# Kernel tuning notes

Measured on AMD Instinct MI355X. Metric: run time of the kernel, lower is better.

Reference implementation:

```python
import jax, jax.numpy as jnp
from jax import lax
import numpy as np

EPS_COS = 1e-8   # cosine-similarity eps (matches F.cosine_similarity default scale)
EPS_IN = 1e-5    # InstanceNorm2d default eps
NEG = -1e9


def _conv3(x, w, b):
    # x: [B,C,H,W], w: [O,I,3,3]
    y = lax.conv_general_dilated(x, w, (1, 1), 'SAME',
                                 dimension_numbers=('NCHW', 'OIHW', 'NCHW'))
    return y + b[None, :, None, None]


def _inorm(x):
    m = jnp.mean(x, axis=(2, 3), keepdims=True)
    v = jnp.var(x, axis=(2, 3), keepdims=True)
    return (x - m) * lax.rsqrt(v + EPS_IN)


def _shift(former, latter, mask):
    # former/latter: [B,C,H,W]; mask: [H,W] int (1 = hole).
    # For every masked pixel, find the most cosine-similar UNMASKED pixel in the
    # latter (known-region encoder) features and copy the former feature from it.
    B, C, H, W = former.shape
    L = H * W
    lat = lax.stop_gradient(latter).reshape(B, C, L)           # attention is non-differentiable
    latn = lat / (jnp.linalg.norm(lat, axis=1, keepdims=True) + EPS_COS)
    sim = jnp.einsum('bcm,bcn->bmn', latn, latn)               # [B,L,L] query m -> key n
    mflat = mask.reshape(L) > 0
    sim = jnp.where(mflat[None, None, :], NEG, sim)            # keys must be unmasked
    idx = jnp.argmax(sim, axis=-1)                             # [B,L]
    fflat = former.reshape(B, C, L)
    gathered = jnp.take_along_axis(fflat, jnp.broadcast_to(idx[:, None, :], (B, C, L)), axis=2)
    shift = jnp.where(mflat[None, None, :], gathered, 0.0)     # zeros outside the hole
    return shift.reshape(B, C, H, W)


def setup_inputs() -> dict:
    key = jax.random.key(0)
    ks = jax.random.split(key, 6)
    B, C, H, W = 8, 256, 64, 64
    inp = jax.random.normal(ks[0], (B, 2 * C, H, W), dtype=jnp.float32)
    mask = jax.random.randint(ks[1], (H, W), 0, 2, dtype=jnp.int32)
    s1 = 1.0 / float(np.sqrt(2 * C * 9))
    s2 = 1.0 / float(np.sqrt(C * 9))
    W1 = jax.random.uniform(ks[2], (C, 2 * C, 3, 3), jnp.float32, -s1, s1)
    b1 = jax.random.uniform(ks[3], (C,), jnp.float32, -s1, s1)
    W2 = jax.random.uniform(ks[4], (C, C, 3, 3), jnp.float32, -s2, s2)
    b2 = jax.random.uniform(ks[5], (C,), jnp.float32, -s2, s2)
    return {"input": inp, "mask": mask, "W1": W1, "b1": b1, "W2": W2, "b2": b2}


def reference(input, mask, W1, b1, W2, b2):
    C = input.shape[1] // 2
    F_c = input[:, :C]          # former (decoder) features
    F_s = input[:, C:]          # latter (encoder) features
    F_shift = _shift(F_c, F_s, mask)
    F_fuse = F_c * F_shift
    F_com = jnp.concatenate([F_c, F_fuse], axis=1)             # [B,2C,H,W]
    h = jax.nn.relu(_inorm(_conv3(F_com, W1, b1)))
    res = _inorm(_conv3(h, W2, b2))
    return jnp.concatenate([F_c + res, F_s], axis=1)
```

## Files before the change

kernel.cpp:

```cpp
#include <hip/hip_runtime.h>
#include <hip/hip_bf16.h>
#include <math.h>

#define L 4096
#define C 256
#define B 8

typedef __attribute__((ext_vector_type(8))) short bf16x8;
typedef __attribute__((ext_vector_type(8))) ushort u16x8;
typedef __attribute__((ext_vector_type(4))) float f32x4;

__device__ inline ushort f2bu(float f) { __hip_bfloat16 h = __float2bfloat16(f); return *(ushort*)&h; }
__device__ inline float bu2f(ushort u) { __hip_bfloat16 h; *(ushort*)&h = u; return __bfloat162float(h); }

__global__ __launch_bounds__(256) void compact_mask(
    const int* __restrict__ mask, int* __restrict__ counts,
    int* __restrict__ maskedOrig, int* __restrict__ unmaskOrig,
    int* __restrict__ posOf)
{
    __shared__ int smM[256], smU[256];
    int t = threadIdx.x;
    int flags[16];
    int cm = 0, cu = 0;
    for (int k = 0; k < 16; ++k) {
        int l = t * 16 + k;
        int f = mask[l] > 0;
        flags[k] = f;
        cm += f; cu += !f;
    }
    smM[t] = cm; smU[t] = cu;
    __syncthreads();
    for (int off = 1; off < 256; off <<= 1) {
        int vM = 0, vU = 0;
        if (t >= off) { vM = smM[t - off]; vU = smU[t - off]; }
        __syncthreads();
        smM[t] += vM; smU[t] += vU;
        __syncthreads();
    }
    if (t == 255) { counts[0] = smM[255]; counts[1] = smU[255]; }
    int pm = smM[t] - cm, pu = smU[t] - cu;
    for (int k = 0; k < 16; ++k) {
        int l = t * 16 + k;
        if (flags[k]) { maskedOrig[pm] = l; posOf[l] = pm; pm++; }
        else          { unmaskOrig[pu] = l; posOf[l] = pu; pu++; }
    }
}

__global__ __launch_bounds__(256) void norm_transpose(
    const float* __restrict__ input, const int* __restrict__ mask,
    const int* __restrict__ counts, const int* __restrict__ posOf,
    ushort* __restrict__ fsnh, ushort* __restrict__ fsnl)
{
    int bx = blockIdx.x;
    int b = bx >> 7;
    int l0 = (bx & 127) * 32;
    __shared__ float tile[256 * 33];
    __shared__ float part[8 * 33];
    __shared__ float denom[32];
    __shared__ int   rowdst[32];
    int t = threadIdx.x;
    int lsub = t & 31, cg = t >> 5;
    for (int cc = 0; cc < 256; cc += 8) {
        int c = cc + cg;
        tile[c * 33 + lsub] = input[((size_t)(b * 512 + 256 + c)) * L + l0 + lsub];
    }
    __syncthreads();
    float s = 0.f;
    for (int c = cg; c < 256; c += 8) { float v = tile[c * 33 + lsub]; s = fmaf(v, v, s); }
    part[cg * 33 + lsub] = s;
    __syncthreads();
    if (t < 32) {
        float s2 = 0.f;
        for (int g = 0; g < 8; ++g) s2 += part[g * 33 + t];
        denom[t] = sqrtf(s2) + 1e-8f;
        int l = l0 + t;
        int Nm = counts[0];
        rowdst[t] = (mask[l] > 0) ? posOf[l] : (Nm + posOf[l]);
    }
    __syncthreads();
    for (int ls = 0; ls < 32; ++ls) {
        int r = rowdst[ls];
        float d = denom[ls];
        float val = tile[t * 33 + ls] / d;
        ushort h = f2bu(val);
        float hf = bu2f(h);
        ushort lo = f2bu(val - hf);
        size_t o = ((size_t)b * L + r) * C + t;
        fsnh[o] = h;
        fsnl[o] = lo;
    }
}

__global__ __launch_bounds__(512, 1) void sim_argmax_v3(
    const ushort* __restrict__ hi, const ushort* __restrict__ lo,
    const int* __restrict__ counts,
    float* __restrict__ pval, int* __restrict__ pidx)
{
    __shared__ ushort ldsB[65536];
    const int Nm = counts[0], Nu = counts[1];
    const int b = blockIdx.z;
    const int m0 = blockIdx.y * 64;
    const int half = blockIdx.x;
    const int t = threadIdx.x;
    const int w = t >> 6, l = t & 63;
    const int lm = l & 15, lk = l >> 4;
    const int mh = w & 1, nq = w >> 1;

    const int nct = (Nu + 63) >> 6;
    const int hs = (nct + 1) >> 1;
    const int cA = half * hs, cB = half ? nct : hs;

    float bestv0[4], bestv1[4]; int bestn0[4], bestn1[4];
#pragma unroll
    for (int r = 0; r < 4; ++r) {
        bestv0[r] = -3e38f; bestn0[r] = 0;
        bestv1[r] = -3e38f; bestn1[r] = 0;
    }

    if (m0 >= Nm) return;

    if (cA < cB) {
        char* ldsc = (char*)ldsB;
        const char* bytesH = (const char*)hi;
        const char* bytesL = (const char*)lo;
        const size_t bL = (size_t)b * L;

#define STAGE(bufofs, cc) do { \
    size_t gb = (bL + (size_t)Nm + (size_t)(cc) * 64) * 512; \
    _Pragma("unroll") \
    for (int i = 0; i < 4; ++i) { \
        int xu = w * 4096 + i * 1024; \
        int xl = xu + l * 16; \
        int sx = xl ^ (((xl >> 9) & 7) << 4); \
        __builtin_amdgcn_global_load_lds((const __attribute__((address_space(1))) unsigned*)(bytesH + gb + sx), \
            (__attribute__((address_space(3))) unsigned*)(ldsc + (bufofs) + xu), 16, 0, 0); \
        __builtin_amdgcn_global_load_lds((const __attribute__((address_space(1))) unsigned*)(bytesL + gb + sx), \
            (__attribute__((address_space(3))) unsigned*)(ldsc + (bufofs) + 32768 + xu), 16, 0, 0); \
    } \
} while (0)

        STAGE(0, cA);

        const int rA0 = m0 + mh * 32 + lm;
        bf16x8 ah0[8], al0[8], ah1[8], al1[8];
        {
            const ushort* aH0 = hi + (bL + rA0) * C + lk * 8;
            const ushort* aL0 = lo + (bL + rA0) * C + lk * 8;
            const ushort* aH1 = aH0 + 16 * C;
            const ushort* aL1 = aL0 + 16 * C;
#pragma unroll
            for (int ks = 0; ks < 8; ++ks) {
                ah0[ks] = *(const bf16x8*)(aH0 + ks * 32);
                al0[ks] = *(const bf16x8*)(aL0 + ks * 32);
                ah1[ks] = *(const bf16x8*)(aH1 + ks * 32);
                al1[ks] = *(const bf16x8*)(aL1 + ks * 32);
            }
        }

        const int row = nq * 16 + lm;
        const int key = (row & 7) << 4;

        for (int c = cA; c < cB; ++c) {
            int bo = ((c - cA) & 1) * 65536;
            asm volatile("s_waitcnt vmcnt(0)" ::: "memory");
            __syncthreads();
            if (c + 1 < cB) STAGE(bo ^ 65536, c + 1);
            const char* bhp = ldsc + bo + row * 512;
            const char* blp = bhp + 32768;
            f32x4 acc0 = (f32x4){0.f, 0.f, 0.f, 0.f};
            f32x4 acc1 = (f32x4){0.f, 0.f, 0.f, 0.f};
#pragma unroll
            for (int ks = 0; ks < 8; ++ks) {
                int off = (ks * 64 + lk * 16) ^ key;
                bf16x8 bh = *(const bf16x8*)(bhp + off);
                bf16x8 bl = *(const bf16x8*)(blp + off);
                acc0 = __builtin_amdgcn_mfma_f32_16x16x32_bf16(ah0[ks], bh, acc0, 0, 0, 0);
                acc0 = __builtin_amdgcn_mfma_f32_16x16x32_bf16(ah0[ks], bl, acc0, 0, 0, 0);
                acc0 = __builtin_amdgcn_mfma_f32_16x16x32_bf16(al0[ks], bh, acc0, 0, 0, 0);
                acc1 = __builtin_amdgcn_mfma_f32_16x16x32_bf16(ah1[ks], bh, acc1, 0, 0, 0);
                acc1 = __builtin_amdgcn_mfma_f32_16x16x32_bf16(ah1[ks], bl, acc1, 0, 0, 0);
                acc1 = __builtin_amdgcn_mfma_f32_16x16x32_bf16(al1[ks], bh, acc1, 0, 0, 0);
            }
            int n = c * 64 + nq * 16 + lm;
            bool nv = n < Nu;
#pragma unroll
            for (int r = 0; r < 4; ++r) {
                float v0 = acc0[r];
                if (nv && v0 > bestv0[r]) { bestv0[r] = v0; bestn0[r] = n; }
                float v1 = acc1[r];
                if (nv && v1 > bestv1[r]) { bestv1[r] = v1; bestn1[r] = n; }
            }
        }
#undef STAGE
    }

#pragma unroll
    for (int r = 0; r < 4; ++r) {
        float bv = bestv0[r]; int bn = bestn0[r];
#pragma unroll
        for (int mk = 1; mk < 16; mk <<= 1) {
            float ov = __shfl_xor(bv, mk, 64);
            int   on = __shfl_xor(bn, mk, 64);
            if (ov > bv || (ov == bv && on < bn)) { bv = ov; bn = on; }
        }
        if (lm == 0) {
            int m = m0 + mh * 32 + lk * 4 + r;
            size_t o = ((size_t)(b * 4096 + m)) * 8 + half * 4 + nq;
            pval[o] = bv; pidx[o] = bn;
        }
        bv = bestv1[r]; bn = bestn1[r];
#pragma unroll
        for (int mk = 1; mk < 16; mk <<= 1) {
            float ov = __shfl_xor(bv, mk, 64);
            int   on = __shfl_xor(bn, mk, 64);
            if (ov > bv || (ov == bv && on < bn)) { bv = ov; bn = on; }
        }
        if (lm == 0) {
            int m = m0 + mh * 32 + 16 + lk * 4 + r;
            size_t o = ((size_t)(b * 4096 + m)) * 8 + half * 4 + nq;
            pval[o] = bv; pidx[o] = bn;
        }
    }
}

__global__ __launch_bounds__(256) void argmax_reduce8(
    const float* __restrict__ pval, const int* __restrict__ pidx,
    const int* __restrict__ counts, const int* __restrict__ maskedOrig,
    const int* __restrict__ unmaskOrig, int* __restrict__ idxmap)
{
    int i = blockIdx.x * 256 + threadIdx.x;
    int b = i >> 12, m = i & 4095;
    if (m >= counts[0]) return;
    size_t base = (size_t)i * 8;
    float bv = pval[base]; int bn = pidx[base];
#pragma unroll
    for (int p = 1; p < 8; ++p) {
        float v = pval[base + p]; int n2 = pidx[base + p];
        if (v > bv || (v == bv && n2 < bn)) { bv = v; bn = n2; }
    }
    idxmap[(b << 12) + maskedOrig[m]] = unmaskOrig[bn];
}

__global__ __launch_bounds__(256) void wprep(
    const float* __restrict__ W1, const float* __restrict__ W2,
    ushort* __restrict__ W1bf, ushort* __restrict__ W2bf)
{
    int gid = blockIdx.x * 256 + threadIdx.x;
    const int N1 = 256 * 512 * 9;
    const int N2 = 256 * 256 * 9;
    if (gid < N1) {
        int ci = gid & 511; int rest = gid >> 9;
        int tau = rest % 9; int co = rest / 9;
        W1bf[gid] = f2bu(W1[((size_t)(co * 512 + ci)) * 9 + tau]);
    } else if (gid < N1 + N2) {
        int g = gid - N1;
        int ci = g & 255; int rest = g >> 8;
        int tau = rest % 9; int co = rest / 9;
        W2bf[g] = f2bu(W2[((size_t)(co * 256 + ci)) * 9 + tau]);
    }
}

__global__ __launch_bounds__(256) void in_prep1(
    const float* __restrict__ input, ushort* __restrict__ inT)
{
    int b = blockIdx.y;
    int p0 = blockIdx.x * 32;
    __shared__ float tile[256][33];
    int t = threadIdx.x;
    int pq = t & 7;
    for (int cc = 0; cc < 256; cc += 32) {
        int ci = cc + (t >> 3);
        float4 v = *(const float4*)(input + ((size_t)(b * 512 + ci)) * L + p0 + pq * 4);
        tile[ci][pq * 4 + 0] = v.x; tile[ci][pq * 4 + 1] = v.y;
        tile[ci][pq * 4 + 2] = v.z; tile[ci][pq * 4 + 3] = v.w;
    }
    __syncthreads();
    int c8 = t & 31;
    for (int pp = 0; pp < 32; pp += 8) {
        int pixloc = pp + (t >> 5);
        u16x8 u;
#pragma unroll
        for (int j = 0; j < 8; ++j) u[j] = f2bu(tile[c8 * 8 + j][pixloc]);
        *(u16x8*)(inT + ((size_t)(b * 4096 + p0 + pixloc)) * 512 + c8 * 8) = u;
    }
}

__global__ __launch_bounds__(256) void in_prep2(
    ushort* __restrict__ inT, const int* __restrict__ mask,
    const int* __restrict__ idxmap)
{
    int gid = blockIdx.x * 256 + threadIdx.x;
    int c8 = gid & 31;
    int pix = (gid >> 5) & 4095;
    int b = gid >> 17;
    u16x8 out8;
    if (mask[pix] > 0) {
        int n = idxmap[(b << 12) + pix];
        const ushort* rp = inT + ((size_t)(b * 4096 + pix)) * 512 + c8 * 8;
        const ushort* rn = inT + ((size_t)(b * 4096 + n)) * 512 + c8 * 8;
        u16x8 a = *(const u16x8*)rp;
        u16x8 bb = *(const u16x8*)rn;
#pragma unroll
        for (int j = 0; j < 8; ++j) out8[j] = f2bu(bu2f(a[j]) * bu2f(bb[j]));
    } else {
#pragma unroll
        for (int j = 0; j < 8; ++j) out8[j] = 0;
    }
    *(u16x8*)(inT + ((size_t)(b * 4096 + pix)) * 512 + 256 + c8 * 8) = out8;
}

template<int CKROW>
__global__ __launch_bounds__(256, 2) void conv_mfma(
    const ushort* __restrict__ Abf, const ushort* __restrict__ Wbf,
    float* __restrict__ outF, ushort* __restrict__ outH,
    float* __restrict__ psum, int store32)
{
    __shared__ float4 ldsv[62208 / 16];
    char* lds = (char*)ldsv;
    char* ldsB = lds + 25344;
    const int t = threadIdx.x;
    const int w = t >> 6;
    const int l = t & 63;
    const int lm = l & 15, lk = l >> 4;
    const int b = blockIdx.z;
    const int y0 = blockIdx.x * 4;
    const int c0 = blockIdx.y * 64;
    const int yw = y0 + w;
    const size_t abase = (size_t)b * 4096 * CKROW;

    f32x4 acc[4][4];
#pragma unroll
    for (int g = 0; g < 4; ++g)
#pragma unroll
        for (int nf = 0; nf < 4; ++nf) acc[g][nf] = (f32x4){0.f, 0.f, 0.f, 0.f};

    if (t < 48) {
        int r = t >> 3;
        int cX = ((t >> 2) & 1) ? 65 : 0;
        int k8 = t & 3;
        *(float4*)(lds + (r * 66 + cX) * 64 + ((k8 * 16) ^ ((cX & 3) << 4))) = (float4){0.f,0.f,0.f,0.f};
    }

    const int NKC = CKROW / 32;
    for (int kc = 0; kc < NKC; ++kc) {
        __syncthreads();
        {
            int x = t >> 2;
            int k8 = t & 3;
            int cX = x + 1;
            char* dbase = lds + cX * 64 + ((k8 * 16) ^ ((cX & 3) << 4));
#pragma unroll
            for (int r = 0; r < 6; ++r) {
                int yy = y0 - 1 + r;
                float4 v;
                if (yy >= 0 && yy < 64)
                    v = *(const float4*)(Abf + abase + (size_t)(yy * 64 + x) * CKROW + kc * 32 + k8 * 8);
                else
                    v = (float4){0.f, 0.f, 0.f, 0.f};
                *(float4*)(dbase + r * (66 * 64)) = v;
            }
        }
        {
            int cl = t >> 2;
            int k8 = t & 3;
            char* dbase = ldsB + cl * 64 + ((k8 * 16) ^ ((cl & 3) << 4));
            const ushort* sbase = Wbf + ((size_t)(c0 + cl) * 9) * CKROW + kc * 32 + k8 * 8;
#pragma unroll
            for (int tau = 0; tau < 9; ++tau) {
                *(float4*)(dbase + tau * (64 * 64)) = *(const float4*)(sbase + (size_t)tau * CKROW);
            }
        }
        __syncthreads();
#pragma unroll
        for (int ky = 0; ky < 3; ++ky) {
            int r = w + ky;
#pragma unroll
            for (int kx = 0; kx < 3; ++kx) {
                int tau = ky * 3 + kx;
                bf16x8 bfr[4];
#pragma unroll
                for (int nf = 0; nf < 4; ++nf) {
                    int cl = nf * 16 + lm;
                    bfr[nf] = *(bf16x8*)(ldsB + (tau * 64 + cl) * 64 + ((lk * 16) ^ ((cl & 3) << 4)));
                }
#pragma unroll
                for (int g = 0; g < 4; ++g) {
                    int cX = g * 16 + lm + kx;
                    bf16x8 afr = *(bf16x8*)(lds + (r * 66 + cX) * 64 + ((lk * 16) ^ ((cX & 3) << 4)));
#pragma unroll
                    for (int nf = 0; nf < 4; ++nf)
                        acc[g][nf] = __builtin_amdgcn_mfma_f32_16x16x32_bf16(afr, bfr[nf], acc[g][nf], 0, 0, 0);
                }
            }
        }
    }

    if (store32) {
#pragma unroll
        for (int g = 0; g < 4; ++g)
#pragma unroll
            for (int nf = 0; nf < 4; ++nf) {
                int cout = c0 + nf * 16 + lm;
#pragma unroll
                for (int r = 0; r < 4; ++r) {
                    int pix = yw * 64 + g * 16 + lk * 4 + r;
                    outF[((size_t)(b * 4096 + pix)) * 256 + cout] = acc[g][nf][r];
                }
            }
    } else {
#pragma unroll
        for (int g = 0; g < 4; ++g)
#pragma unroll
            for (int nf = 0; nf < 4; ++nf) {
                int cout = c0 + nf * 16 + lm;
#pragma unroll
                for (int r = 0; r < 4; ++r) {
                    int pix = yw * 64 + g * 16 + lk * 4 + r;
                    outH[((size_t)(b * 4096 + pix)) * 256 + cout] = f2bu(acc[g][nf][r]);
                }
            }
    }

    float s[4], q[4];
#pragma unroll
    for (int nf = 0; nf < 4; ++nf) {
        float ss = 0.f, qq = 0.f;
#pragma unroll
        for (int g = 0; g < 4; ++g)
#pragma unroll
            for (int r = 0; r < 4; ++r) { float v = acc[g][nf][r]; ss += v; qq = fmaf(v, v, qq); }
        ss += __shfl_xor(ss, 16, 64); ss += __shfl_xor(ss, 32, 64);
        qq += __shfl_xor(qq, 16, 64); qq += __shfl_xor(qq, 32, 64);
        s[nf] = ss; q[nf] = qq;
    }
    __syncthreads();
    float* S = (float*)lds;
    float* Q = (float*)(lds + 1024);
    if (l < 16) {
#pragma unroll
        for (int nf = 0; nf < 4; ++nf) {
            S[w * 64 + nf * 16 + l] = s[nf];
            Q[w * 64 + nf * 16 + l] = q[nf];
        }
    }
    __syncthreads();
    if (t < 64) {
        float ts = 0.f, tq = 0.f;
#pragma unroll
        for (int w2 = 0; w2 < 4; ++w2) { ts += S[w2 * 64 + t]; tq += Q[w2 * 64 + t]; }
        size_t o = (((size_t)(b * 256 + c0 + t)) * 16 + blockIdx.x) * 2;
        psum[o] = ts; psum[o + 1] = tq;
    }
}

__global__ __launch_bounds__(256) void stats_reduce(
    const float* __restrict__ psum, float* __restrict__ mrs)
{
    int b = blockIdx.x;
    int c = threadIdx.x;
    float s = 0.f, q = 0.f;
    size_t base = ((size_t)(b * 256 + c)) * 16;
    for (int k = 0; k < 16; ++k) { s += psum[(base + k) * 2]; q += psum[(base + k) * 2 + 1]; }
    float mean = s * (1.f / 4096.f);
    float var = q * (1.f / 4096.f) - mean * mean;
    float rs = rsqrtf(var + 1e-5f);
    mrs[(b * 256 + c) * 2] = mean;
    mrs[(b * 256 + c) * 2 + 1] = rs;
}

__global__ __launch_bounds__(256) void norm1_apply(
    const ushort* __restrict__ hraw, const float* __restrict__ mrs,
    ushort* __restrict__ hbf)
{
    int gid = blockIdx.x * 256 + threadIdx.x;
    int c8 = gid & 31;
    int pix = (gid >> 5) & 4095;
    int b = gid >> 17;
    size_t off = (((size_t)(b * 4096 + pix)) << 8) + c8 * 8;
    u16x8 v = *(const u16x8*)(hraw + off);
    const float* mb = mrs + (size_t)b * 512 + c8 * 16;
    u16x8 o;
#pragma unroll
    for (int j = 0; j < 8; ++j) {
        float z = (bu2f(v[j]) - mb[j * 2]) * mb[j * 2 + 1];
        o[j] = f2bu(z > 0.f ? z : 0.f);
    }
    *(u16x8*)(hbf + off) = o;
}

__global__ __launch_bounds__(256) void finalize(
    const ushort* __restrict__ resbf, const float* __restrict__ mrs,
    const float* __restrict__ input, float* __restrict__ out)
{
    int b = blockIdx.y;
    int p0 = blockIdx.x * 32;
    __shared__ float tileT[256][33];
    int t = threadIdx.x;
    int c8 = t & 31;
    for (int pp = 0; pp < 32; pp += 8) {
        int pixloc = pp + (t >> 5);
        u16x8 u = *(const u16x8*)(resbf + (((size_t)(b * 4096 + p0 + pixloc)) << 8) + c8 * 8);
#pragma unroll
        for (int j = 0; j < 8; ++j) tileT[c8 * 8 + j][pixloc] = bu2f(u[j]);
    }
    __syncthreads();
    int pq = t & 7;
    for (int cc = 0; cc < 256; cc += 32) {
        int c = cc + (t >> 3);
        float m = mrs[(b * 256 + c) * 2];
        float rs = mrs[(b * 256 + c) * 2 + 1];
        size_t off = ((size_t)(b * 512 + c)) * L + p0 + pq * 4;
        float4 f = *(const float4*)(input + off);
        float4 o;
        o.x = f.x + (tileT[c][pq * 4 + 0] - m) * rs;
        o.y = f.y + (tileT[c][pq * 4 + 1] - m) * rs;
        o.z = f.z + (tileT[c][pq * 4 + 2] - m) * rs;
        o.w = f.w + (tileT[c][pq * 4 + 3] - m) * rs;
        *(float4*)(out + off) = o;
    }
}

__global__ __launch_bounds__(256) void copy_fs(
    const float* __restrict__ input, float* __restrict__ out)
{
    size_t i = (size_t)blockIdx.x * 256 + threadIdx.x;
    size_t b = i >> 18;
    size_t r = i & 262143;
    size_t o = ((size_t)(b * 512 + 256)) * 1024 + r;
    const float4* s = (const float4*)input;
    float4* d = (float4*)out;
    d[o] = s[o];
}

extern "C" void kernel_launch(void* const* d_in, const int* in_sizes, int n_in,
                              void* d_out, int out_size, void* d_ws, size_t ws_size,
                              hipStream_t stream) {
    const float* input = (const float*)d_in[0];
    const int*   mask  = (const int*)d_in[1];
    const float* W1    = (const float*)d_in[2];
    const float* W2    = (const float*)d_in[4];
    float* out = (float*)d_out;
    (void)in_sizes; (void)n_in; (void)out_size; (void)ws_size;

    char* ob = (char*)d_out;
    char* wp = (char*)d_ws;

    ushort* fsnh = (ushort*)ob;
    ushort* fsnl = (ushort*)(ob + 16777216);
    float*  pval = (float*)(ob + 33554432);
    int*    pidx = (int*)(ob + 37748736);
    ushort* inT  = (ushort*)ob;
    ushort* hraw = (ushort*)(ob + 33554432);
    ushort* hbf  = (ushort*)ob;

    ushort* resbf  = (ushort*)wp;
    ushort* W1bf   = (ushort*)(wp + 16777216);
    ushort* W2bf   = (ushort*)(wp + 19136512);
    float*  psum1  = (float*)(wp + 20316160);
    float*  psum2  = (float*)(wp + 20578304);
    float*  mrs1   = (float*)(wp + 20840448);
    float*  mrs2   = (float*)(wp + 20856832);
    int* counts     = (int*)(wp + 20873216);
    int* maskedOrig = counts + 4;
    int* unmaskOrig = maskedOrig + L;
    int* posOf      = unmaskOrig + L;
    int* idxmap     = posOf + L;

    compact_mask<<<1, 256, 0, stream>>>(mask, counts, maskedOrig, unmaskOrig, posOf);
    norm_transpose<<<1024, 256, 0, stream>>>(input, mask, counts, posOf, fsnh, fsnl);
    sim_argmax_v3<<<dim3(2, 64, 8), 512, 0, stream>>>(fsnh, fsnl, counts, pval, pidx);
    argmax_reduce8<<<128, 256, 0, stream>>>(pval, pidx, counts, maskedOrig, unmaskOrig, idxmap);
    wprep<<<6912, 256, 0, stream>>>(W1, W2, W1bf, W2bf);
    in_prep1<<<dim3(128, 8), 256, 0, stream>>>(input, inT);
    in_prep2<<<4096, 256, 0, stream>>>(inT, mask, idxmap);
    conv_mfma<512><<<dim3(16, 4, 8), 256, 0, stream>>>(inT, W1bf, (float*)nullptr, hraw, psum1, 0);
    stats_reduce<<<8, 256, 0, stream>>>(psum1, mrs1);
    norm1_apply<<<4096, 256, 0, stream>>>(hraw, mrs1, hbf);
    conv_mfma<256><<<dim3(16, 4, 8), 256, 0, stream>>>(hbf, W2bf, (float*)nullptr, resbf, psum2, 0);
    stats_reduce<<<8, 256, 0, stream>>>(psum2, mrs2);
    finalize<<<dim3(128, 8), 256, 0, stream>>>(resbf, mrs2, input, out);
    copy_fs<<<8192, 256, 0, stream>>>(input, out);
}
```

Before: 293.8 us.

## Restructure similarity argmax to 32x32x16 MFMA tiles with 128-row blocks

Rewrites the similarity/argmax kernel so each wave computes a 32x32 tile with the 32x32x16 bf16 MFMA, holding 32 query rows of the hi/lo split in registers. Blocks now cover 128 query rows with 256 threads, split the key range across 4 blocks instead of 2, and stage 32-key tiles in a smaller LDS double buffer so two blocks can share a CU. The partial-argmax reduction is shrunk from 8 to 4 candidates to match. This aims to cut LDS traffic per MFMA and raise occupancy, at the cost of higher register pressure from 16 accumulator and 16 best-value slots per lane.

```diff
diff --git a/kernel.cpp b/kernel.cpp
--- a/kernel.cpp
+++ b/kernel.cpp
@@ -9,6 +9,7 @@
 typedef __attribute__((ext_vector_type(8))) short bf16x8;
 typedef __attribute__((ext_vector_type(8))) ushort u16x8;
 typedef __attribute__((ext_vector_type(4))) float f32x4;
+typedef __attribute__((ext_vector_type(16))) float f32x16;
 
 __device__ inline ushort f2bu(float f) { __hip_bfloat16 h = __float2bfloat16(f); return *(ushort*)&h; }
 __device__ inline float bu2f(ushort u) { __hip_bfloat16 h; *(ushort*)&h = u; return __bfloat162float(h); }
@@ -91,139 +92,110 @@
     }
 }
 
-__global__ __launch_bounds__(512, 1) void sim_argmax_v3(
+__global__ __launch_bounds__(256, 2) void sim_argmax_v4(
     const ushort* __restrict__ hi, const ushort* __restrict__ lo,
     const int* __restrict__ counts,
     float* __restrict__ pval, int* __restrict__ pidx)
 {
-    __shared__ ushort ldsB[65536];
+    __shared__ ushort ldsB[32768];
     const int Nm = counts[0], Nu = counts[1];
     const int b = blockIdx.z;
-    const int m0 = blockIdx.y * 64;
-    const int half = blockIdx.x;
+    const int m0 = blockIdx.y * 128;
+    const int nq = blockIdx.x;
+    if (m0 >= Nm) return;
     const int t = threadIdx.x;
     const int w = t >> 6, l = t & 63;
-    const int lm = l & 15, lk = l >> 4;
-    const int mh = w & 1, nq = w >> 1;
-
-    const int nct = (Nu + 63) >> 6;
-    const int hs = (nct + 1) >> 1;
-    const int cA = half * hs, cB = half ? nct : hs;
-
-    float bestv0[4], bestv1[4]; int bestn0[4], bestn1[4];
-#pragma unroll
-    for (int r = 0; r < 4; ++r) {
-        bestv0[r] = -3e38f; bestn0[r] = 0;
-        bestv1[r] = -3e38f; bestn1[r] = 0;
-    }
-
-    if (m0 >= Nm) return;
-
-    if (cA < cB) {
+    const int col = l & 31, kh = l >> 5;
+    const int key = (col & 7) << 4;
+
+    const int nct = (Nu + 31) >> 5;
+    const int q0 = (nq * nct) >> 2;
+    const int q1 = ((nq + 1) * nct) >> 2;
+
+    float bestv[16]; int bestn[16];
+#pragma unroll
+    for (int q = 0; q < 16; ++q) { bestv[q] = -3e38f; bestn[q] = 0; }
+
+    if (q0 < q1) {
         char* ldsc = (char*)ldsB;
         const char* bytesH = (const char*)hi;
         const char* bytesL = (const char*)lo;
         const size_t bL = (size_t)b * L;
 
 #define STAGE(bufofs, cc) do { \
-    size_t gb = (bL + (size_t)Nm + (size_t)(cc) * 64) * 512; \
+    size_t gb = (bL + (size_t)Nm + (size_t)(cc) * 32) * 512; \
     _Pragma("unroll") \
     for (int i = 0; i < 4; ++i) { \
-        int xu = w * 4096 + i * 1024; \
-        int xl = xu + l * 16; \
-        int sx = xl ^ (((xl >> 9) & 7) << 4); \
+        int x = i * 4096 + t * 16; \
+        int sx = x ^ (((x >> 9) & 7) << 4); \
         __builtin_amdgcn_global_load_lds((const __attribute__((address_space(1))) unsigned*)(bytesH + gb + sx), \
-            (__attribute__((address_space(3))) unsigned*)(ldsc + (bufofs) + xu), 16, 0, 0); \
+            (__attribute__((address_space(3))) unsigned*)(ldsc + (bufofs) + x), 16, 0, 0); \
         __builtin_amdgcn_global_load_lds((const __attribute__((address_space(1))) unsigned*)(bytesL + gb + sx), \
-            (__attribute__((address_space(3))) unsigned*)(ldsc + (bufofs) + 32768 + xu), 16, 0, 0); \
+            (__attribute__((address_space(3))) unsigned*)(ldsc + (bufofs) + 16384 + x), 16, 0, 0); \
     } \
 } while (0)
 
-        STAGE(0, cA);
-
-        const int rA0 = m0 + mh * 32 + lm;
-        bf16x8 ah0[8], al0[8], ah1[8], al1[8];
+        STAGE(0, q0);
+
+        const int rA = m0 + w * 32 + col;
+        bf16x8 ah[16], al[16];
         {
-            const ushort* aH0 = hi + (bL + rA0) * C + lk * 8;
-            const ushort* aL0 = lo + (bL + rA0) * C + lk * 8;
-            const ushort* aH1 = aH0 + 16 * C;
-            const ushort* aL1 = aL0 + 16 * C;
-#pragma unroll
-            for (int ks = 0; ks < 8; ++ks) {
-                ah0[ks] = *(const bf16x8*)(aH0 + ks * 32);
-                al0[ks] = *(const bf16x8*)(aL0 + ks * 32);
-                ah1[ks] = *(const bf16x8*)(aH1 + ks * 32);
-                al1[ks] = *(const bf16x8*)(aL1 + ks * 32);
-            }
-        }
-
-        const int row = nq * 16 + lm;
-        const int key = (row & 7) << 4;
-
-        for (int c = cA; c < cB; ++c) {
-            int bo = ((c - cA) & 1) * 65536;
+            const ushort* aH = hi + (bL + rA) * C + kh * 8;
+            const ushort* aL = lo + (bL + rA) * C + kh * 8;
+#pragma unroll
+            for (int ks = 0; ks < 16; ++ks) {
+                ah[ks] = *(const bf16x8*)(aH + ks * 16);
+                al[ks] = *(const bf16x8*)(aL + ks * 16);
+            }
+        }
+
+        for (int c = q0; c < q1; ++c) {
+            int bo = ((c - q0) & 1) * 16384;
+            int bob = ((c - q0) & 1) * 32768;
+            (void)bo;
             asm volatile("s_waitcnt vmcnt(0)" ::: "memory");
             __syncthreads();
-            if (c + 1 < cB) STAGE(bo ^ 65536, c + 1);
-            const char* bhp = ldsc + bo + row * 512;
-            const char* blp = bhp + 32768;
-            f32x4 acc0 = (f32x4){0.f, 0.f, 0.f, 0.f};
-            f32x4 acc1 = (f32x4){0.f, 0.f, 0.f, 0.f};
-#pragma unroll
-            for (int ks = 0; ks < 8; ++ks) {
-                int off = (ks * 64 + lk * 16) ^ key;
-                bf16x8 bh = *(const bf16x8*)(bhp + off);
-                bf16x8 bl = *(const bf16x8*)(blp + off);
-                acc0 = __builtin_amdgcn_mfma_f32_16x16x32_bf16(ah0[ks], bh, acc0, 0, 0, 0);
-                acc0 = __builtin_amdgcn_mfma_f32_16x16x32_bf16(ah0[ks], bl, acc0, 0, 0, 0);
-                acc0 = __builtin_amdgcn_mfma_f32_16x16x32_bf16(al0[ks], bh, acc0, 0, 0, 0);
-                acc1 = __builtin_amdgcn_mfma_f32_16x16x32_bf16(ah1[ks], bh, acc1, 0, 0, 0);
-                acc1 = __builtin_amdgcn_mfma_f32_16x16x32_bf16(ah1[ks], bl, acc1, 0, 0, 0);
-                acc1 = __builtin_amdgcn_mfma_f32_16x16x32_bf16(al1[ks], bh, acc1, 0, 0, 0);
-            }
-            int n = c * 64 + nq * 16 + lm;
+            if (c + 1 < q1) STAGE(bob ^ 32768, c + 1);
+            f32x16 acc = (f32x16){0.f,0.f,0.f,0.f,0.f,0.f,0.f,0.f,0.f,0.f,0.f,0.f,0.f,0.f,0.f,0.f};
+            const char* cbase = ldsc + bob + col * 512;
+#pragma unroll
+            for (int ks = 0; ks < 16; ++ks) {
+                int off = (ks * 32 + kh * 16) ^ key;
+                bf16x8 bh = *(const bf16x8*)(cbase + off);
+                bf16x8 bl = *(const bf16x8*)(cbase + 16384 + off);
+                acc = __builtin_amdgcn_mfma_f32_32x32x16_bf16(ah[ks], bh, acc, 0, 0, 0);
+                acc = __builtin_amdgcn_mfma_f32_32x32x16_bf16(ah[ks], bl, acc, 0, 0, 0);
+                acc = __builtin_amdgcn_mfma_f32_32x32x16_bf16(al[ks], bh, acc, 0, 0, 0);
+            }
+            int n = c * 32 + col;
             bool nv = n < Nu;
 #pragma unroll
-            for (int r = 0; r < 4; ++r) {
-                float v0 = acc0[r];
-                if (nv && v0 > bestv0[r]) { bestv0[r] = v0; bestn0[r] = n; }
-                float v1 = acc1[r];
-                if (nv && v1 > bestv1[r]) { bestv1[r] = v1; bestn1[r] = n; }
+            for (int q = 0; q < 16; ++q) {
+                float v = acc[q];
+                if (nv && v > bestv[q]) { bestv[q] = v; bestn[q] = n; }
             }
         }
 #undef STAGE
     }
 
 #pragma unroll
-    for (int r = 0; r < 4; ++r) {
-        float bv = bestv0[r]; int bn = bestn0[r];
-#pragma unroll
-        for (int mk = 1; mk < 16; mk <<= 1) {
+    for (int q = 0; q < 16; ++q) {
+        float bv = bestv[q]; int bn = bestn[q];
+#pragma unroll
+        for (int mk = 1; mk < 32; mk <<= 1) {
             float ov = __shfl_xor(bv, mk, 64);
             int   on = __shfl_xor(bn, mk, 64);
             if (ov > bv || (ov == bv && on < bn)) { bv = ov; bn = on; }
         }
-        if (lm == 0) {
-            int m = m0 + mh * 32 + lk * 4 + r;
-            size_t o = ((size_t)(b * 4096 + m)) * 8 + half * 4 + nq;
+        if (col == 0) {
+            int m = m0 + w * 32 + (q & 3) + 8 * (q >> 2) + 4 * kh;
+            size_t o = ((size_t)(b * 4096 + m)) * 4 + nq;
             pval[o] = bv; pidx[o] = bn;
         }
-        bv = bestv1[r]; bn = bestn1[r];
-#pragma unroll
-        for (int mk = 1; mk < 16; mk <<= 1) {
-            float ov = __shfl_xor(bv, mk, 64);
-            int   on = __shfl_xor(bn, mk, 64);
-            if (ov > bv || (ov == bv && on < bn)) { bv = ov; bn = on; }
-        }
-        if (lm == 0) {
-            int m = m0 + mh * 32 + 16 + lk * 4 + r;
-            size_t o = ((size_t)(b * 4096 + m)) * 8 + half * 4 + nq;
-            pval[o] = bv; pidx[o] = bn;
-        }
-    }
-}
-
-__global__ __launch_bounds__(256) void argmax_reduce8(
+    }
+}
+
+__global__ __launch_bounds__(256) void argmax_reduce4(
     const float* __restrict__ pval, const int* __restrict__ pidx,
     const int* __restrict__ counts, const int* __restrict__ maskedOrig,
     const int* __restrict__ unmaskOrig, int* __restrict__ idxmap)
@@ -231,10 +203,10 @@
     int i = blockIdx.x * 256 + threadIdx.x;
     int b = i >> 12, m = i & 4095;
     if (m >= counts[0]) return;
-    size_t base = (size_t)i * 8;
+    size_t base = (size_t)i * 4;
     float bv = pval[base]; int bn = pidx[base];
 #pragma unroll
-    for (int p = 1; p < 8; ++p) {
+    for (int p = 1; p < 4; ++p) {
         float v = pval[base + p]; int n2 = pidx[base + p];
         if (v > bv || (v == bv && n2 < bn)) { bv = v; bn = n2; }
     }
@@ -568,8 +540,8 @@
 
     compact_mask<<<1, 256, 0, stream>>>(mask, counts, maskedOrig, unmaskOrig, posOf);
     norm_transpose<<<1024, 256, 0, stream>>>(input, mask, counts, posOf, fsnh, fsnl);
-    sim_argmax_v3<<<dim3(2, 64, 8), 512, 0, stream>>>(fsnh, fsnl, counts, pval, pidx);
-    argmax_reduce8<<<128, 256, 0, stream>>>(pval, pidx, counts, maskedOrig, unmaskOrig, idxmap);
+    sim_argmax_v4<<<dim3(4, 32, 8), 256, 0, stream>>>(fsnh, fsnl, counts, pval, pidx);
+    argmax_reduce4<<<128, 256, 0, stream>>>(pval, pidx, counts, maskedOrig, unmaskOrig, idxmap);
     wprep<<<6912, 256, 0, stream>>>(W1, W2, W1bf, W2bf);
     in_prep1<<<dim3(128, 8), 256, 0, stream>>>(input, inT);
     in_prep2<<<4096, 256, 0, stream>>>(inT, mask, idxmap);
```

Result: faster. 283.0 us (-3.7%).
